# Performance work log

Hardware: AMD Instinct MI355X
Metric: run time of the kernel (lower is better)

## Reference

```python
import jax, jax.numpy as jnp
import numpy as np

NB, B, IN, HID = 8, 256, 512, 512
G = 4 * HID
WB, IB, ABNM = 8, 8, 8
NL = 0.05


def quant(x, bits, r):
    # QuantFunc.forward: scale, clamp to (-1+1/step, 1-1/step), round to step grid, rescale
    step = 2.0 ** (bits - 1)
    x01 = jnp.clip(x / r, -1.0 + 1.0 / step, 1.0 - 1.0 / step)
    return jnp.round(x01 * step) / step * r


def pact(x, a):
    # pact_a_bmm vectorized over the block dim: sign(x)*0.5*(|x| - ||x|-a| + a)
    a3 = a[:, None, None]
    return jnp.sign(x) * 0.5 * (jnp.abs(x) - jnp.abs(jnp.abs(x) - a3) + a3)


def custom_mm(inp, w, b, nw, nb):
    # CustomMM_bmm.forward: quantize weights/bias (range 1.0), add scaled noise, bmm
    wq = quant(w, WB, 1.0)
    bq = quant(b, WB, 1.0)
    out = jnp.einsum('bni,bio->bno', inp, wq + nw * jnp.max(w) * NL)
    return out + bq + nb * jnp.max(b) * NL


def setup_inputs():
    key = jax.random.key(0)
    ks = jax.random.split(key, 11)
    inp = {
        'input': jax.random.normal(ks[0], (B, IN), jnp.float32),
        'hx': jax.random.normal(ks[1], (NB, B, HID), jnp.float32),
        'cx': jax.random.normal(ks[2], (NB, B, HID), jnp.float32),
        'weight_ih': jax.random.normal(ks[3], (NB, IN, G), jnp.float32),
        'weight_hh': jax.random.normal(ks[4], (NB, HID, G), jnp.float32),
        'bias_ih': jax.random.normal(ks[5], (NB, 1, G), jnp.float32),
        'bias_hh': jax.random.normal(ks[6], (NB, 1, G), jnp.float32),
        'noise_wih': jax.random.normal(ks[7], (NB, IN, G), jnp.float32),
        'noise_whh': jax.random.normal(ks[8], (NB, HID, G), jnp.float32),
        'noise_bih': jax.random.normal(ks[9], (NB, 1, G), jnp.float32),
        'noise_bhh': jax.random.normal(ks[10], (NB, 1, G), jnp.float32),
        'a1': jnp.full((NB,), 128.0, jnp.float32),
        'a3': jnp.ones((NB,), jnp.float32),
        'a4': jnp.ones((NB,), jnp.float32),
        'a5': jnp.ones((NB,), jnp.float32),
        'a6': jnp.ones((NB,), jnp.float32),
        'a7': jnp.full((NB,), 4.0, jnp.float32),
        'a8': jnp.ones((NB,), jnp.float32),
        'a9': jnp.full((NB,), 4.0, jnp.float32),
        'a10': jnp.ones((NB,), jnp.float32),
        'a11': jnp.full((NB,), 4.0, jnp.float32),
    }
    return inp


def reference(input, hx, cx, weight_ih, weight_hh, bias_ih, bias_hh,
              noise_wih, noise_whh, noise_bih, noise_bhh,
              a1, a3, a4, a5, a6, a7, a8, a9, a10, a11):
    xr = jnp.broadcast_to(input[None], (NB,) + input.shape)  # input.repeat(n_blocks,1,1)
    xq = quant(pact(xr, a1), IB, a1[:, None, None])
    gates = custom_mm(xq, weight_ih, bias_ih, noise_wih, noise_bih) \
          + custom_mm(hx, weight_hh, bias_hh, noise_whh, noise_bhh)
    i, j, f, o = jnp.split(gates, 4, axis=2)
    qp = lambda x, a: quant(pact(x, a), ABNM, a[:, None, None])
    fg = qp(jax.nn.sigmoid(f), a3)
    ig = qp(jax.nn.sigmoid(i), a4)
    act = qp(jnp.tanh(j), a5)
    og = qp(jax.nn.sigmoid(o), a6)
    gated = qp(cx * fg, a7)
    actin = qp(ig * act, a8)
    new_c = qp(gated + actin, a9)
    actc = qp(jnp.tanh(new_c), a10)
    new_h = qp(actc * og, a11)
    return new_h, new_c
```

## Files before the change

kernel.cpp:

```cpp
#include <hip/hip_runtime.h>
#include <hip/hip_bf16.h>

#define NBATCH 8
#define BROWS 256
#define KDIM 512
#define HIDD 512
#define GDIM 2048
#define KSTEP 64
#define NIT (KDIM / KSTEP)

typedef float f32x4 __attribute__((ext_vector_type(4)));
typedef __bf16 bf16x8 __attribute__((ext_vector_type(8)));

__device__ __forceinline__ unsigned fenc(float f) {
    unsigned u = __float_as_uint(f);
    return (u & 0x80000000u) ? ~u : (u | 0x80000000u);
}
__device__ __forceinline__ float fdec(unsigned e) {
    unsigned u = (e & 0x80000000u) ? (e & 0x7fffffffu) : ~e;
    return __uint_as_float(u);
}
__device__ __forceinline__ unsigned umaxu(unsigned a, unsigned b) { return a > b ? a : b; }

__device__ __forceinline__ float qpact(float x, float a) {
    float ax = fabsf(x);
    float p  = copysignf(0.5f * (ax - fabsf(ax - a) + a), x);
    float x01 = p / a;
    x01 = fminf(fmaxf(x01, -0.9921875f), 0.9921875f);
    return (rintf(x01 * 128.f) * 0.0078125f) * a;
}
__device__ __forceinline__ float q1(float x) {
    float x01 = fminf(fmaxf(x, -0.9921875f), 0.9921875f);
    return rintf(x01 * 128.f) * 0.0078125f;
}
__device__ __forceinline__ float sigmf(float x) { return 1.0f / (1.0f + expf(-x)); }

__global__ void k_max(const float* __restrict__ w_ih, const float* __restrict__ w_hh,
                      const float* __restrict__ b_ih, const float* __restrict__ b_hh,
                      unsigned* __restrict__ omax) {
    int which = blockIdx.y;
    const float* src = which == 0 ? w_ih : which == 1 ? w_hh : which == 2 ? b_ih : b_hh;
    int n4 = (which < 2 ? NBATCH * KDIM * GDIM : NBATCH * GDIM) >> 2;
    unsigned best = 0u;
    int stride = gridDim.x * blockDim.x;
    for (int i = blockIdx.x * blockDim.x + threadIdx.x; i < n4; i += stride) {
        float4 v = ((const float4*)src)[i];
        best = umaxu(best, fenc(v.x)); best = umaxu(best, fenc(v.y));
        best = umaxu(best, fenc(v.z)); best = umaxu(best, fenc(v.w));
    }
    #pragma unroll
    for (int off = 32; off > 0; off >>= 1)
        best = umaxu(best, (unsigned)__shfl_down((int)best, off, 64));
    __shared__ unsigned red[4];
    int lane = threadIdx.x & 63, wv = threadIdx.x >> 6;
    if (lane == 0) red[wv] = best;
    __syncthreads();
    if (threadIdx.x == 0) {
        unsigned b2 = umaxu(umaxu(red[0], red[1]), umaxu(red[2], red[3]));
        atomicMax(&omax[which], b2);
    }
}

__global__ void k_prep(const float* __restrict__ input, const float* __restrict__ hx,
                       const float* __restrict__ bih, const float* __restrict__ bhh,
                       const float* __restrict__ nbih, const float* __restrict__ nbhh,
                       const float* __restrict__ a1, const unsigned* __restrict__ maxes,
                       __hip_bfloat16* __restrict__ xqh, __hip_bfloat16* __restrict__ hxh,
                       __hip_bfloat16* __restrict__ hxl, float* __restrict__ bias_comb) {
    const int NX = NBATCH * BROWS * KDIM;
    const int NH = NBATCH * BROWS * HIDD;
    const int NBC = NBATCH * GDIM;
    int total = NX + NH + NBC;
    int stride = gridDim.x * blockDim.x;
    for (int i = blockIdx.x * blockDim.x + threadIdx.x; i < total; i += stride) {
        if (i < NX) {
            int nb = i >> 17;
            int rem = i & 131071;
            float v = qpact(input[rem], a1[nb]);
            xqh[i] = __float2bfloat16(v);
        } else if (i < NX + NH) {
            int j = i - NX;
            float h = hx[j];
            __hip_bfloat16 hi = __float2bfloat16(h);
            hxh[j] = hi;
            hxl[j] = __float2bfloat16(h - __bfloat162float(hi));
        } else {
            int j = i - NX - NH;
            float mb_ih = fdec(maxes[2]);
            float mb_hh = fdec(maxes[3]);
            bias_comb[j] = q1(bih[j]) + (nbih[j] * mb_ih) * 0.05f
                         + q1(bhh[j]) + (nbhh[j] * mb_hh) * 0.05f;
        }
    }
}

__global__ __launch_bounds__(1024, 1) void k_gemm(
    const float* __restrict__ w_ih, const float* __restrict__ w_hh,
    const float* __restrict__ n_ih, const float* __restrict__ n_hh,
    const __hip_bfloat16* __restrict__ xqh, const __hip_bfloat16* __restrict__ hxh,
    const __hip_bfloat16* __restrict__ hxl,
    const float* __restrict__ bias_comb,
    const unsigned* __restrict__ maxes,
    float* __restrict__ gates)
{
    __shared__ __hip_bfloat16 Bsm[2][4][64][72];

    int tid = threadIdx.x;
    int lane = tid & 63, wv = tid >> 6;
    int nb = blockIdx.x & 7;
    int gc = blockIdx.x >> 3;

    const float* wih_b = w_ih + nb * KDIM * GDIM;
    const float* whh_b = w_hh + nb * KDIM * GDIM;
    const float* nih_b = n_ih + nb * KDIM * GDIM;
    const float* nhh_b = n_hh + nb * KDIM * GDIM;
    const __hip_bfloat16* xq_b = xqh + nb * BROWS * KDIM;
    const __hip_bfloat16* hh_b = hxh + nb * BROWS * KDIM;
    const __hip_bfloat16* hl_b = hxl + nb * BROWS * KDIM;

    float c_ih = fdec(maxes[0]);
    float c_hh = fdec(maxes[1]);

    f32x4 acc[4] = {};

    int lh = lane & 15;
    int g  = lane >> 4;
    int arow = (wv << 4) + lh;

    int sn   = tid & 63;
    int soct = (tid >> 6) & 7;
    int shh  = tid >> 9;
    const float* wsrc = shh ? whh_b : wih_b;
    const float* zsrc = shh ? nhh_b : nih_b;
    float cmax = shh ? c_hh : c_ih;
    int matHi = shh << 1;
    int scol = (gc << 6) + sn;

    float rwa[8], rza[8], rwb[8], rzb[8];
    bf16x8 ax0, ax1, ah0, ah1, al0, al1;

#define STAGE(RW, RZ, K0) {                                  \
    int kb = (K0) + (soct << 3);                             \
    _Pragma("unroll")                                        \
    for (int j = 0; j < 8; ++j) {                            \
        int gx = (kb + j) * GDIM + scol;                     \
        RW[j] = wsrc[gx]; RZ[j] = zsrc[gx];                  \
    } }

#define ALOAD(K0) {                                          \
    int a0 = arow * KDIM + (K0) + (g << 3);                  \
    ax0 = *(const bf16x8*)(xq_b + a0);                       \
    ax1 = *(const bf16x8*)(xq_b + a0 + 32);                  \
    ah0 = *(const bf16x8*)(hh_b + a0);                       \
    ah1 = *(const bf16x8*)(hh_b + a0 + 32);                  \
    al0 = *(const bf16x8*)(hl_b + a0);                       \
    al1 = *(const bf16x8*)(hl_b + a0 + 32);                  \
    }

#define CVT(P, RW, RZ) {                                     \
    bf16x8 hi8, lo8;                                         \
    _Pragma("unroll")                                        \
    for (int j = 0; j < 8; ++j) {                            \
        float w = RW[j];                                     \
        float wq = rintf(fminf(fmaxf(w, -0.9921875f), 0.9921875f) * 128.f) * 0.0078125f; \
        float e = wq + (RZ[j] * cmax) * 0.05f;               \
        __hip_bfloat16 h = __float2bfloat16(e);              \
        float lo = e - __bfloat162float(h);                  \
        __hip_bfloat16 l = __float2bfloat16(lo);             \
        hi8[j] = *reinterpret_cast<__bf16*>(&h);             \
        lo8[j] = *reinterpret_cast<__bf16*>(&l);             \
    }                                                        \
    *(bf16x8*)&Bsm[P][matHi][sn][soct << 3] = hi8;           \
    *(bf16x8*)&Bsm[P][matHi + 1][sn][soct << 3] = lo8; }

#define COMPUTE(P) {                                         \
    _Pragma("unroll")                                        \
    for (int nf = 0; nf < 4; ++nf) {                         \
        int n = (nf << 4) + lh;                              \
        int kb0 = g << 3, kb1 = 32 + kb0;                    \
        bf16x8 b0 = *(const bf16x8*)&Bsm[P][0][n][kb0];      \
        bf16x8 b1 = *(const bf16x8*)&Bsm[P][1][n][kb0];      \
        bf16x8 b2 = *(const bf16x8*)&Bsm[P][2][n][kb0];      \
        bf16x8 b3 = *(const bf16x8*)&Bsm[P][3][n][kb0];      \
        acc[nf] = __builtin_amdgcn_mfma_f32_16x16x32_bf16(ax0, b0, acc[nf], 0, 0, 0); \
        acc[nf] = __builtin_amdgcn_mfma_f32_16x16x32_bf16(ax0, b1, acc[nf], 0, 0, 0); \
        acc[nf] = __builtin_amdgcn_mfma_f32_16x16x32_bf16(ah0, b2, acc[nf], 0, 0, 0); \
        acc[nf] = __builtin_amdgcn_mfma_f32_16x16x32_bf16(ah0, b3, acc[nf], 0, 0, 0); \
        acc[nf] = __builtin_amdgcn_mfma_f32_16x16x32_bf16(al0, b2, acc[nf], 0, 0, 0); \
        b0 = *(const bf16x8*)&Bsm[P][0][n][kb1];             \
        b1 = *(const bf16x8*)&Bsm[P][1][n][kb1];             \
        b2 = *(const bf16x8*)&Bsm[P][2][n][kb1];             \
        b3 = *(const bf16x8*)&Bsm[P][3][n][kb1];             \
        acc[nf] = __builtin_amdgcn_mfma_f32_16x16x32_bf16(ax1, b0, acc[nf], 0, 0, 0); \
        acc[nf] = __builtin_amdgcn_mfma_f32_16x16x32_bf16(ax1, b1, acc[nf], 0, 0, 0); \
        acc[nf] = __builtin_amdgcn_mfma_f32_16x16x32_bf16(ah1, b2, acc[nf], 0, 0, 0); \
        acc[nf] = __builtin_amdgcn_mfma_f32_16x16x32_bf16(ah1, b3, acc[nf], 0, 0, 0); \
        acc[nf] = __builtin_amdgcn_mfma_f32_16x16x32_bf16(al1, b2, acc[nf], 0, 0, 0); \
    } }

    STAGE(rwa, rza, 0);
    STAGE(rwb, rzb, KSTEP);

    for (int it = 0; it < NIT; it += 2) {
        ALOAD(it * KSTEP);
        CVT(0, rwa, rza);
        if (it + 2 < NIT) STAGE(rwa, rza, (it + 2) * KSTEP);
        __syncthreads();
        COMPUTE(0);
        ALOAD((it + 1) * KSTEP);
        CVT(1, rwb, rzb);
        if (it + 3 < NIT) STAGE(rwb, rzb, (it + 3) * KSTEP);
        __syncthreads();
        COMPUTE(1);
    }

    #pragma unroll
    for (int nf = 0; nf < 4; ++nf) {
        int gcol = (gc << 6) + (nf << 4) + lh;
        float bc = bias_comb[nb * GDIM + gcol];
        #pragma unroll
        for (int rg = 0; rg < 4; ++rg) {
            int r = (wv << 4) + (g << 2) + rg;
            gates[((nb * BROWS + r) * GDIM) + gcol] = acc[nf][rg] + bc;
        }
    }
}

__global__ __launch_bounds__(512) void k_cell(
    const float* __restrict__ gates, const float* __restrict__ cx,
    const float* __restrict__ a3, const float* __restrict__ a4, const float* __restrict__ a5,
    const float* __restrict__ a6, const float* __restrict__ a7, const float* __restrict__ a8,
    const float* __restrict__ a9, const float* __restrict__ a10, const float* __restrict__ a11,
    float* __restrict__ out_h, float* __restrict__ out_c)
{
    int idx = blockIdx.x * blockDim.x + threadIdx.x;
    int nb = idx >> 15;
    int rem = idx & 32767;
    const float* gb = gates + (size_t)(nb * BROWS * GDIM) + rem * 4
                    - (rem >> 7) * 2048 + (rem >> 7) * 2048;
    int row = rem >> 7;
    int hq  = rem & 127;
    const float* gr = gates + ((size_t)(nb * BROWS + row) * GDIM) + hq * 4;
    f32x4 gi = *(const f32x4*)(gr);
    f32x4 gj = *(const f32x4*)(gr + 512);
    f32x4 gf = *(const f32x4*)(gr + 1024);
    f32x4 go = *(const f32x4*)(gr + 1536);
    int oidx = (nb * BROWS + row) * HIDD + hq * 4;
    f32x4 cv = *(const f32x4*)(cx + oidx);
    float A3 = a3[nb], A4 = a4[nb], A5 = a5[nb], A6 = a6[nb], A7 = a7[nb];
    float A8 = a8[nb], A9 = a9[nb], A10 = a10[nb], A11 = a11[nb];
    f32x4 nh, nc;
    #pragma unroll
    for (int j = 0; j < 4; ++j) {
        float fg = qpact(sigmf(gf[j]), A3);
        float ig = qpact(sigmf(gi[j]), A4);
        float act = qpact(tanhf(gj[j]), A5);
        float og = qpact(sigmf(go[j]), A6);
        float gated = qpact(cv[j] * fg, A7);
        float actin = qpact(ig * act, A8);
        float ncv = qpact(gated + actin, A9);
        float acv = qpact(tanhf(ncv), A10);
        nh[j] = qpact(acv * og, A11);
        nc[j] = ncv;
    }
    *(f32x4*)(out_h + oidx) = nh;
    *(f32x4*)(out_c + oidx) = nc;
}

extern "C" void kernel_launch(void* const* d_in, const int* in_sizes, int n_in,
                              void* d_out, int out_size, void* d_ws, size_t ws_size,
                              hipStream_t stream) {
    const float* input = (const float*)d_in[0];
    const float* hx    = (const float*)d_in[1];
    const float* cx    = (const float*)d_in[2];
    const float* w_ih  = (const float*)d_in[3];
    const float* w_hh  = (const float*)d_in[4];
    const float* b_ih  = (const float*)d_in[5];
    const float* b_hh  = (const float*)d_in[6];
    const float* n_wih = (const float*)d_in[7];
    const float* n_whh = (const float*)d_in[8];
    const float* n_bih = (const float*)d_in[9];
    const float* n_bhh = (const float*)d_in[10];
    const float* a1  = (const float*)d_in[11];
    const float* a3  = (const float*)d_in[12];
    const float* a4  = (const float*)d_in[13];
    const float* a5  = (const float*)d_in[14];
    const float* a6  = (const float*)d_in[15];
    const float* a7  = (const float*)d_in[16];
    const float* a8  = (const float*)d_in[17];
    const float* a9  = (const float*)d_in[18];
    const float* a10 = (const float*)d_in[19];
    const float* a11 = (const float*)d_in[20];

    float* out_h = (float*)d_out;
    float* out_c = out_h + NBATCH * BROWS * HIDD;

    char* ws = (char*)d_ws;
    unsigned* maxes = (unsigned*)ws;
    __hip_bfloat16* xqh = (__hip_bfloat16*)(ws + 256);
    __hip_bfloat16* hxh = (__hip_bfloat16*)(ws + 256 + 2097152);
    __hip_bfloat16* hxl = (__hip_bfloat16*)(ws + 256 + 2 * 2097152);
    float* bias_comb    = (float*)(ws + 256 + 3 * 2097152);
    float* gates        = (float*)(ws + 256 + 3 * 2097152 + 65536);

    hipMemsetAsync(maxes, 0, 32, stream);
    k_max<<<dim3(256, 4), 256, 0, stream>>>(w_ih, w_hh, b_ih, b_hh, maxes);
    k_prep<<<2048, 256, 0, stream>>>(input, hx, b_ih, b_hh, n_bih, n_bhh, a1, maxes,
                                     xqh, hxh, hxl, bias_comb);
    k_gemm<<<NBATCH * 32, 1024, 0, stream>>>(w_ih, w_hh, n_wih, n_whh, xqh, hxh, hxl,
                                             bias_comb, maxes, gates);
    k_cell<<<512, 512, 0, stream>>>(gates, cx, a3, a4, a5, a6, a7, a8, a9, a10, a11,
                                    out_h, out_c);
}
```

Measured before the change: 83.29 us.

## Switch GEMM to 32x32x16 MFMA with k-major LDS layout

Replaces the 16x16x32 bf16 MFMA tiling (each wave 16 rows x 64 cols, four accumulators) with 32x32x16 MFMA where each wave owns a 32x32 tile and a single 16-register accumulator. The shared-memory B buffer is changed to a k-octet-major layout of bf16x8 vectors, which removes the padding and is meant to make the per-lane LDS reads contiguous. The barrier is also moved ahead of the next global prefetch, and an unused pointer computation in the cell kernel is removed. The aim is fewer LDS reads per MFMA and better MFMA throughput. The cost is that the A fragment loads from global memory become smaller 16-element strided chunks, and more A registers are live.

```diff
diff --git a/kernel.cpp b/kernel.cpp
--- a/kernel.cpp
+++ b/kernel.cpp
@@ -10,6 +10,7 @@
 #define NIT (KDIM / KSTEP)
 
 typedef float f32x4 __attribute__((ext_vector_type(4)));
+typedef float f32x16 __attribute__((ext_vector_type(16)));
 typedef __bf16 bf16x8 __attribute__((ext_vector_type(8)));
 
 __device__ __forceinline__ unsigned fenc(float f) {
@@ -103,7 +104,7 @@
     const unsigned* __restrict__ maxes,
     float* __restrict__ gates)
 {
-    __shared__ __hip_bfloat16 Bsm[2][4][64][72];
+    __shared__ bf16x8 Bsm[2][4][8][64];
 
     int tid = threadIdx.x;
     int lane = tid & 63, wv = tid >> 6;
@@ -121,11 +122,14 @@
     float c_ih = fdec(maxes[0]);
     float c_hh = fdec(maxes[1]);
 
-    f32x4 acc[4] = {};
-
-    int lh = lane & 15;
-    int g  = lane >> 4;
-    int arow = (wv << 4) + lh;
+    f32x16 acc = {};
+
+    int l31 = lane & 31;
+    int khalf = lane >> 5;
+    int band = wv & 7;
+    int ch = wv >> 3;
+    int arow = band * 32 + l31;
+    int nidx = ch * 32 + l31;
 
     int sn   = tid & 63;
     int soct = (tid >> 6) & 7;
@@ -137,7 +141,7 @@
     int scol = (gc << 6) + sn;
 
     float rwa[8], rza[8], rwb[8], rzb[8];
-    bf16x8 ax0, ax1, ah0, ah1, al0, al1;
+    bf16x8 ax[4], ah[4], al[4];
 
 #define STAGE(RW, RZ, K0) {                                  \
     int kb = (K0) + (soct << 3);                             \
@@ -148,14 +152,13 @@
     } }
 
 #define ALOAD(K0) {                                          \
-    int a0 = arow * KDIM + (K0) + (g << 3);                  \
-    ax0 = *(const bf16x8*)(xq_b + a0);                       \
-    ax1 = *(const bf16x8*)(xq_b + a0 + 32);                  \
-    ah0 = *(const bf16x8*)(hh_b + a0);                       \
-    ah1 = *(const bf16x8*)(hh_b + a0 + 32);                  \
-    al0 = *(const bf16x8*)(hl_b + a0);                       \
-    al1 = *(const bf16x8*)(hl_b + a0 + 32);                  \
-    }
+    _Pragma("unroll")                                        \
+    for (int kc = 0; kc < 4; ++kc) {                         \
+        int off = arow * KDIM + (K0) + (kc << 4) + (khalf << 3); \
+        ax[kc] = *(const bf16x8*)(xq_b + off);               \
+        ah[kc] = *(const bf16x8*)(hh_b + off);               \
+        al[kc] = *(const bf16x8*)(hl_b + off);               \
+    } }
 
 #define CVT(P, RW, RZ) {                                     \
     bf16x8 hi8, lo8;                                         \
@@ -170,32 +173,22 @@
         hi8[j] = *reinterpret_cast<__bf16*>(&h);             \
         lo8[j] = *reinterpret_cast<__bf16*>(&l);             \
     }                                                        \
-    *(bf16x8*)&Bsm[P][matHi][sn][soct << 3] = hi8;           \
-    *(bf16x8*)&Bsm[P][matHi + 1][sn][soct << 3] = lo8; }
+    Bsm[P][matHi][soct][sn] = hi8;                           \
+    Bsm[P][matHi + 1][soct][sn] = lo8; }
+
+#define MFMA(A, B) acc = __builtin_amdgcn_mfma_f32_32x32x16_bf16(A, B, acc, 0, 0, 0)
 
 #define COMPUTE(P) {                                         \
     _Pragma("unroll")                                        \
-    for (int nf = 0; nf < 4; ++nf) {                         \
-        int n = (nf << 4) + lh;                              \
-        int kb0 = g << 3, kb1 = 32 + kb0;                    \
-        bf16x8 b0 = *(const bf16x8*)&Bsm[P][0][n][kb0];      \
-        bf16x8 b1 = *(const bf16x8*)&Bsm[P][1][n][kb0];      \
-        bf16x8 b2 = *(const bf16x8*)&Bsm[P][2][n][kb0];      \
-        bf16x8 b3 = *(const bf16x8*)&Bsm[P][3][n][kb0];      \
-        acc[nf] = __builtin_amdgcn_mfma_f32_16x16x32_bf16(ax0, b0, acc[nf], 0, 0, 0); \
-        acc[nf] = __builtin_amdgcn_mfma_f32_16x16x32_bf16(ax0, b1, acc[nf], 0, 0, 0); \
-        acc[nf] = __builtin_amdgcn_mfma_f32_16x16x32_bf16(ah0, b2, acc[nf], 0, 0, 0); \
-        acc[nf] = __builtin_amdgcn_mfma_f32_16x16x32_bf16(ah0, b3, acc[nf], 0, 0, 0); \
-        acc[nf] = __builtin_amdgcn_mfma_f32_16x16x32_bf16(al0, b2, acc[nf], 0, 0, 0); \
-        b0 = *(const bf16x8*)&Bsm[P][0][n][kb1];             \
-        b1 = *(const bf16x8*)&Bsm[P][1][n][kb1];             \
-        b2 = *(const bf16x8*)&Bsm[P][2][n][kb1];             \
-        b3 = *(const bf16x8*)&Bsm[P][3][n][kb1];             \
-        acc[nf] = __builtin_amdgcn_mfma_f32_16x16x32_bf16(ax1, b0, acc[nf], 0, 0, 0); \
-        acc[nf] = __builtin_amdgcn_mfma_f32_16x16x32_bf16(ax1, b1, acc[nf], 0, 0, 0); \
-        acc[nf] = __builtin_amdgcn_mfma_f32_16x16x32_bf16(ah1, b2, acc[nf], 0, 0, 0); \
-        acc[nf] = __builtin_amdgcn_mfma_f32_16x16x32_bf16(ah1, b3, acc[nf], 0, 0, 0); \
-        acc[nf] = __builtin_amdgcn_mfma_f32_16x16x32_bf16(al1, b2, acc[nf], 0, 0, 0); \
+    for (int kc = 0; kc < 4; ++kc) {                         \
+        int ko = (kc << 1) + khalf;                          \
+        bf16x8 b0 = Bsm[P][0][ko][nidx];                     \
+        bf16x8 b1 = Bsm[P][1][ko][nidx];                     \
+        bf16x8 b2 = Bsm[P][2][ko][nidx];                     \
+        bf16x8 b3 = Bsm[P][3][ko][nidx];                     \
+        MFMA(ax[kc], b0); MFMA(ax[kc], b1);                  \
+        MFMA(ah[kc], b2); MFMA(ah[kc], b3);                  \
+        MFMA(al[kc], b2);                                    \
     } }
 
     STAGE(rwa, rza, 0);
@@ -204,25 +197,23 @@
     for (int it = 0; it < NIT; it += 2) {
         ALOAD(it * KSTEP);
         CVT(0, rwa, rza);
+        __syncthreads();
         if (it + 2 < NIT) STAGE(rwa, rza, (it + 2) * KSTEP);
-        __syncthreads();
         COMPUTE(0);
         ALOAD((it + 1) * KSTEP);
         CVT(1, rwb, rzb);
+        __syncthreads();
         if (it + 3 < NIT) STAGE(rwb, rzb, (it + 3) * KSTEP);
-        __syncthreads();
         COMPUTE(1);
     }
 
+    int gcol = (gc << 6) + (ch << 5) + l31;
+    float bc = bias_comb[nb * GDIM + gcol];
     #pragma unroll
-    for (int nf = 0; nf < 4; ++nf) {
-        int gcol = (gc << 6) + (nf << 4) + lh;
-        float bc = bias_comb[nb * GDIM + gcol];
-        #pragma unroll
-        for (int rg = 0; rg < 4; ++rg) {
-            int r = (wv << 4) + (g << 2) + rg;
-            gates[((nb * BROWS + r) * GDIM) + gcol] = acc[nf][rg] + bc;
-        }
+    for (int reg = 0; reg < 16; ++reg) {
+        int row = (reg & 3) + 8 * (reg >> 2) + 4 * khalf;
+        int grow = band * 32 + row;
+        gates[((nb * BROWS + grow) * GDIM) + gcol] = acc[reg] + bc;
     }
 }
 
@@ -236,8 +227,6 @@
     int idx = blockIdx.x * blockDim.x + threadIdx.x;
     int nb = idx >> 15;
     int rem = idx & 32767;
-    const float* gb = gates + (size_t)(nb * BROWS * GDIM) + rem * 4
-                    - (rem >> 7) * 2048 + (rem >> 7) * 2048;
     int row = rem >> 7;
     int hq  = rem & 127;
     const float* gr = gates + ((size_t)(nb * BROWS + row) * GDIM) + hq * 4;
```

Measured after the change: 107.6 us. +29.2%, slower.
